# Optimization experiments

Hardware: AMD Instinct MI355X
Metric: run time of the kernel (lower is better)

The kernel has to match this reference:

```python
import jax, jax.numpy as jnp
import numpy as np

BATCH = 4096
FILTER_NUM = 1024
REL_CNT = 19
REL_DIM = 1024


def setup_inputs() -> dict:
    key = jax.random.key(0)
    k1, k2, k3 = jax.random.split(key, 3)
    conv_output = jax.random.normal(k1, (BATCH, FILTER_NUM, REL_CNT), dtype=jnp.float32)
    R_output = jax.random.normal(k2, (REL_CNT, REL_DIM), dtype=jnp.float32)
    # U ~ truncated_normal(stddev=0.1); plain normal*0.1 is an acceptable init stand-in
    U = jax.random.normal(k3, (FILTER_NUM, REL_DIM), dtype=jnp.float32) * 0.1
    return {"conv_output": conv_output, "R_output": R_output, "U": U}


def reference(conv_output, R_output, U):
    # Original: for each relation r, score[:, r] = conv_output[:, :, r] @ U @ R_output[r, :]
    # Batched as a single einsum: scores[b, r] = sum_{f,e} conv[b,f,r] * U[f,e] * R[r,e]
    # Contract the large f axis first (GEMM-dominant), then reduce over e per relation.
    proj = jnp.einsum('bfr,fe->bre', conv_output, U)      # [B, R, E]
    scores = jnp.einsum('bre,re->br', proj, R_output)     # [B, R]
    return scores
```

## Files before the change

### kernel.cpp

```cpp
#include <hip/hip_runtime.h>

#define BATCH      4096
#define FILTER_NUM 1024
#define REL_CNT    19
#define REL_DIM    1024
#define SLAB       (FILTER_NUM * REL_CNT)
#define ITERS      (SLAB / (256 * 4))

__global__ __launch_bounds__(256) void compute_V_kernel(
        const float* __restrict__ U,
        const float* __restrict__ Rm,
        float* __restrict__ V)
{
    const int f   = blockIdx.x;
    const int tid = threadIdx.x;

    float acc[REL_CNT];
#pragma unroll
    for (int r = 0; r < REL_CNT; ++r) acc[r] = 0.0f;

    const float* __restrict__ Urow = U + (size_t)f * REL_DIM;
    for (int e = tid; e < REL_DIM; e += 256) {
        const float u = Urow[e];
#pragma unroll
        for (int r = 0; r < REL_CNT; ++r)
            acc[r] = fmaf(u, Rm[r * REL_DIM + e], acc[r]);
    }

    __shared__ float s[4][REL_CNT];
    const int lane = tid & 63;
    const int wave = tid >> 6;
#pragma unroll
    for (int r = 0; r < REL_CNT; ++r) {
        float v = acc[r];
#pragma unroll
        for (int off = 32; off > 0; off >>= 1)
            v += __shfl_down(v, off, 64);
        if (lane == 0) s[wave][r] = v;
    }
    __syncthreads();
    if (tid < REL_CNT)
        V[f * REL_CNT + tid] = s[0][tid] + s[1][tid] + s[2][tid] + s[3][tid];
}

__global__ __launch_bounds__(256) void score_kernel(
        const float* __restrict__ conv,
        const float* __restrict__ V,
        float* __restrict__ out)
{
    const int b   = blockIdx.x;
    const int tid = threadIdx.x;

    const float4* __restrict__ c4 = (const float4*)(conv + (size_t)b * SLAB);
    const float4* __restrict__ v4 = (const float4*)V;

    const int o = (4 * tid) % REL_CNT;

    float acc[REL_CNT];
#pragma unroll
    for (int j = 0; j < REL_CNT; ++j) acc[j] = 0.0f;

#pragma unroll
    for (int iter = 0; iter < ITERS; ++iter) {
        const int idx = iter * 256 + tid;
        const float4 c = c4[idx];
        const float4 v = v4[idx];
        acc[(17 * iter + 0) % REL_CNT] = fmaf(c.x, v.x, acc[(17 * iter + 0) % REL_CNT]);
        acc[(17 * iter + 1) % REL_CNT] = fmaf(c.y, v.y, acc[(17 * iter + 1) % REL_CNT]);
        acc[(17 * iter + 2) % REL_CNT] = fmaf(c.z, v.z, acc[(17 * iter + 2) % REL_CNT]);
        acc[(17 * iter + 3) % REL_CNT] = fmaf(c.w, v.w, acc[(17 * iter + 3) % REL_CNT]);
    }

    __shared__ float s[256 * REL_CNT];
#pragma unroll
    for (int j = 0; j < REL_CNT; ++j) {
        int r = o + j;
        if (r >= REL_CNT) r -= REL_CNT;
        s[tid * REL_CNT + r] = acc[j];
    }
    __syncthreads();

    __shared__ float s2[8 * REL_CNT];
    if (tid < 8 * REL_CNT) {
        const int r = tid % REL_CNT;
        const int g = tid / REL_CNT;
        float sum = 0.0f;
#pragma unroll
        for (int i = 0; i < 32; ++i)
            sum += s[(g * 32 + i) * REL_CNT + r];
        s2[g * REL_CNT + r] = sum;
    }
    __syncthreads();

    if (tid < REL_CNT) {
        float sum = 0.0f;
#pragma unroll
        for (int g = 0; g < 8; ++g)
            sum += s2[g * REL_CNT + tid];
        out[b * REL_CNT + tid] = sum;
    }
}

extern "C" void kernel_launch(void* const* d_in, const int* in_sizes, int n_in,
                              void* d_out, int out_size, void* d_ws, size_t ws_size,
                              hipStream_t stream) {
    const float* conv = (const float*)d_in[0];
    const float* Rm   = (const float*)d_in[1];
    const float* U    = (const float*)d_in[2];
    float*       out  = (float*)d_out;
    float*       V    = (float*)d_ws;

    compute_V_kernel<<<FILTER_NUM, 256, 0, stream>>>(U, Rm, V);
    score_kernel<<<BATCH, 256, 0, stream>>>(conv, V, out);
}
```

Before: 429.0 us.

## Process four batch rows per block and use nontemporal loads for conv

Each score block now handles four batch rows at once, so each V vector load is reused across four conv slabs, and the grid shrinks by four. The conv loads use nontemporal hints because they are streamed once. In exchange, register pressure quadruples (76 accumulators per thread), which may lower occupancy, and the shared-memory reduction is serialized four times per block.

```diff
diff --git a/kernel.cpp b/kernel.cpp
--- a/kernel.cpp
+++ b/kernel.cpp
@@ -6,6 +6,9 @@
 #define REL_DIM    1024
 #define SLAB       (FILTER_NUM * REL_CNT)
 #define ITERS      (SLAB / (256 * 4))
+#define SPB        4
+
+typedef float vf4 __attribute__((ext_vector_type(4)));
 
 __global__ __launch_bounds__(256) void compute_V_kernel(
         const float* __restrict__ U,
@@ -48,56 +51,69 @@
         const float* __restrict__ V,
         float* __restrict__ out)
 {
-    const int b   = blockIdx.x;
+    const int b0  = blockIdx.x * SPB;
     const int tid = threadIdx.x;
 
-    const float4* __restrict__ c4 = (const float4*)(conv + (size_t)b * SLAB);
-    const float4* __restrict__ v4 = (const float4*)V;
+    const vf4* __restrict__ c4 = (const vf4*)(conv + (size_t)b0 * SLAB);
+    const vf4* __restrict__ v4 = (const vf4*)V;
 
     const int o = (4 * tid) % REL_CNT;
 
-    float acc[REL_CNT];
+    float acc[SPB][REL_CNT];
 #pragma unroll
-    for (int j = 0; j < REL_CNT; ++j) acc[j] = 0.0f;
+    for (int m = 0; m < SPB; ++m)
+#pragma unroll
+        for (int j = 0; j < REL_CNT; ++j) acc[m][j] = 0.0f;
 
 #pragma unroll
     for (int iter = 0; iter < ITERS; ++iter) {
         const int idx = iter * 256 + tid;
-        const float4 c = c4[idx];
-        const float4 v = v4[idx];
-        acc[(17 * iter + 0) % REL_CNT] = fmaf(c.x, v.x, acc[(17 * iter + 0) % REL_CNT]);
-        acc[(17 * iter + 1) % REL_CNT] = fmaf(c.y, v.y, acc[(17 * iter + 1) % REL_CNT]);
-        acc[(17 * iter + 2) % REL_CNT] = fmaf(c.z, v.z, acc[(17 * iter + 2) % REL_CNT]);
-        acc[(17 * iter + 3) % REL_CNT] = fmaf(c.w, v.w, acc[(17 * iter + 3) % REL_CNT]);
+        const vf4 v = v4[idx];
+        vf4 x[SPB];
+#pragma unroll
+        for (int m = 0; m < SPB; ++m)
+            x[m] = __builtin_nontemporal_load(&c4[idx + m * (SLAB / 4)]);
+        const int j0 = (17 * iter + 0) % REL_CNT;
+        const int j1 = (17 * iter + 1) % REL_CNT;
+        const int j2 = (17 * iter + 2) % REL_CNT;
+        const int j3 = (17 * iter + 3) % REL_CNT;
+#pragma unroll
+        for (int m = 0; m < SPB; ++m) {
+            acc[m][j0] = fmaf(x[m].x, v.x, acc[m][j0]);
+            acc[m][j1] = fmaf(x[m].y, v.y, acc[m][j1]);
+            acc[m][j2] = fmaf(x[m].z, v.z, acc[m][j2]);
+            acc[m][j3] = fmaf(x[m].w, v.w, acc[m][j3]);
+        }
     }
 
     __shared__ float s[256 * REL_CNT];
+    __shared__ float s2[8 * REL_CNT];
+
 #pragma unroll
-    for (int j = 0; j < REL_CNT; ++j) {
-        int r = o + j;
-        if (r >= REL_CNT) r -= REL_CNT;
-        s[tid * REL_CNT + r] = acc[j];
-    }
-    __syncthreads();
-
-    __shared__ float s2[8 * REL_CNT];
-    if (tid < 8 * REL_CNT) {
-        const int r = tid % REL_CNT;
-        const int g = tid / REL_CNT;
-        float sum = 0.0f;
+    for (int m = 0; m < SPB; ++m) {
+        if (m > 0) __syncthreads();
 #pragma unroll
-        for (int i = 0; i < 32; ++i)
-            sum += s[(g * 32 + i) * REL_CNT + r];
-        s2[g * REL_CNT + r] = sum;
-    }
-    __syncthreads();
-
-    if (tid < REL_CNT) {
-        float sum = 0.0f;
+        for (int j = 0; j < REL_CNT; ++j) {
+            int r = o + j; if (r >= REL_CNT) r -= REL_CNT;
+            s[tid * REL_CNT + r] = acc[m][j];
+        }
+        __syncthreads();
+        if (tid < 8 * REL_CNT) {
+            const int r = tid % REL_CNT;
+            const int g = tid / REL_CNT;
+            float sum = 0.0f;
 #pragma unroll
-        for (int g = 0; g < 8; ++g)
-            sum += s2[g * REL_CNT + tid];
-        out[b * REL_CNT + tid] = sum;
+            for (int i = 0; i < 32; ++i)
+                sum += s[(g * 32 + i) * REL_CNT + r];
+            s2[g * REL_CNT + r] = sum;
+        }
+        __syncthreads();
+        if (tid < REL_CNT) {
+            float sum = 0.0f;
+#pragma unroll
+            for (int g = 0; g < 8; ++g) sum += s2[g * REL_CNT + tid];
+            out[(b0 + m) * REL_CNT + tid] = sum;
+        }
     }
 }
 
@@ -111,5 +127,5 @@
     float*       V    = (float*)d_ws;
 
     compute_V_kernel<<<FILTER_NUM, 256, 0, stream>>>(U, Rm, V);
-    score_kernel<<<BATCH, 256, 0, stream>>>(conv, V, out);
+    score_kernel<<<BATCH / SPB, 256, 0, stream>>>(conv, V, out);
 }
```

After: 411.6 us. -4.1%, faster.
